# Performance work log

Hardware: AMD Instinct MI355X
Metric: run time of the kernel (lower is better)

The kernel has to match this reference:

```python
import jax, jax.numpy as jnp
import numpy as np

B, E, F, Q = 8, 2000, 6000, 20
D = 256   # entity_dim == word_dim (required: word_embedding output feeds LSTM with input_size=word_dim)
WD = 256
L = 3
NUM_ENTITY, NUM_REL, NUM_WORD = 400000, 6000, 60000
NNZ = 2 * B * F
PAGERANK_LAMBDA, FACT_SCALE = 0.8, 3.0
VERY_NEG = -100000000000.0
VERY_SMALL = 1e-10


def _lin(x, W, b):
    return x @ W.T + b


def _sparse_bmm(indices, values, x, num_rows):
    # indices: [3, nnz] = (batch, row, col); x: [B, C, Dx] -> out [B, num_rows, Dx]
    b, r, c = indices[0], indices[1], indices[2]
    contrib = values[:, None] * x[b, c]
    seg = b * num_rows + r
    out = jax.ops.segment_sum(contrib, seg, num_segments=x.shape[0] * num_rows)
    return out.reshape(x.shape[0], num_rows, x.shape[2])


def _lstm(x, Wih, Whh, bih, bhh):
    # PyTorch LSTM, batch_first, 1 layer, unidirectional; gate order i,f,g,o
    Bb, T, _ = x.shape
    H = Whh.shape[1]
    def step(carry, xt):
        h, c = carry
        g = xt @ Wih.T + bih + h @ Whh.T + bhh
        i, f, gg, o = jnp.split(g, 4, axis=-1)
        c = jax.nn.sigmoid(f) * c + jax.nn.sigmoid(i) * jnp.tanh(gg)
        h = jax.nn.sigmoid(o) * jnp.tanh(c)
        return (h, c), h
    init = (jnp.zeros((Bb, H), x.dtype), jnp.zeros((Bb, H), x.dtype))
    (h, c), hs = jax.lax.scan(step, init, jnp.swapaxes(x, 0, 1))
    return jnp.swapaxes(hs, 0, 1), h


def setup_inputs():
    key = jax.random.key(0)
    ks = iter(jax.random.split(key, 48))
    p = lambda shape: jax.random.normal(next(ks), shape, jnp.float32) * 0.02
    inp = {}
    inp['local_entity'] = jax.random.randint(next(ks), (B, E), 0, NUM_ENTITY + 1)
    inp['q2e_adj_mat'] = (jax.random.uniform(next(ks), (B, E, 1)) < 0.01).astype(jnp.float32)
    inp['kb_fact_rel'] = jax.random.randint(next(ks), (B, F), 0, NUM_REL)
    inp['query_text'] = jax.random.randint(next(ks), (B, Q), 0, NUM_WORD)
    inp['answer_dist'] = (jax.random.uniform(next(ks), (B, E)) < 0.005).astype(jnp.float32)
    eb = jax.random.randint(next(ks), (NNZ,), 0, B)
    ef = jax.random.randint(next(ks), (NNZ,), 0, F)
    ee = jax.random.randint(next(ks), (NNZ,), 0, E)
    inp['e2f_indices'] = jnp.stack([eb, ef, ee])
    inp['e2f_val'] = jnp.ones((NNZ,), jnp.float32)
    fb = jax.random.randint(next(ks), (NNZ,), 0, B)
    fe = jax.random.randint(next(ks), (NNZ,), 0, E)
    ff = jax.random.randint(next(ks), (NNZ,), 0, F)
    inp['f2e_indices'] = jnp.stack([fb, fe, ff])
    inp['f2e_val'] = jnp.ones((NNZ,), jnp.float32)
    inp['entity_table'] = p((NUM_ENTITY + 1, WD)).at[-1].set(0.0)
    inp['ent_lin_W'] = p((D, WD)); inp['ent_lin_b'] = jnp.zeros((D,), jnp.float32)
    inp['relation_table'] = p((NUM_REL + 1, WD)).at[-1].set(0.0)
    inp['rel_lin_W'] = p((D, WD)); inp['rel_lin_b'] = jnp.zeros((D,), jnp.float32)
    inp['word_table'] = p((NUM_WORD + 1, D)).at[-1].set(0.0)
    inp['lstm_Wih'] = p((4 * D, WD)); inp['lstm_Whh'] = p((4 * D, D))
    inp['lstm_bih'] = jnp.zeros((4 * D,), jnp.float32); inp['lstm_bhh'] = jnp.zeros((4 * D,), jnp.float32)
    inp['q2e_W'] = p((L, D, D)); inp['q2e_b'] = jnp.zeros((L, D), jnp.float32)
    inp['e2q_W'] = p((L, D, 3 * D)); inp['e2q_b'] = jnp.zeros((L, D), jnp.float32)
    inp['e2e_W'] = p((L, D, 3 * D)); inp['e2e_b'] = jnp.zeros((L, D), jnp.float32)
    inp['head_W'] = p((L, D, D)); inp['head_b'] = jnp.zeros((L, D), jnp.float32)
    inp['tail_W'] = p((L, D, D)); inp['tail_b'] = jnp.zeros((L, D), jnp.float32)
    inp['self_W'] = p((L, D, D)); inp['self_b'] = jnp.zeros((L, D), jnp.float32)
    inp['score_W'] = p((1, D)); inp['score_b'] = jnp.zeros((1,), jnp.float32)
    return inp


def reference(local_entity, q2e_adj_mat, kb_fact_rel, query_text, answer_dist, e2f_indices, e2f_val, f2e_indices, f2e_val, entity_table, ent_lin_W, ent_lin_b, relation_table, rel_lin_W, rel_lin_b, word_table, lstm_Wih, lstm_Whh, lstm_bih, lstm_bhh, q2e_W, q2e_b, e2q_W, e2q_b, e2e_W, e2e_b, head_W, head_b, tail_W, tail_b, self_W, self_b, score_W, score_b):
    query_mask = (query_text != NUM_WORD).astype(jnp.float32)          # [B,Q]
    local_entity_mask = (local_entity != NUM_ENTITY).astype(jnp.float32)
    # query encoder (dropout = identity in eval)
    query_hidden, h_last = _lstm(word_table[query_text], lstm_Wih, lstm_Whh, lstm_bih, lstm_bhh)
    query_node_emb = h_last[:, None, :]                                # [B,1,D]
    local_fact_emb = _lin(relation_table[kb_fact_rel], rel_lin_W, rel_lin_b)  # [B,F,D]
    div = jnp.sqrt(jnp.float32(D))
    sim = jnp.einsum('bqd,bfd->bqf', query_hidden, local_fact_emb) / div
    sim = jax.nn.softmax(sim + (1.0 - query_mask)[:, :, None] * VERY_NEG, axis=1)
    att = jnp.einsum('bqf,bqd->bfd', sim, query_hidden)
    Wt = jnp.sum(att * local_fact_emb, axis=2) / div                   # [B,F]
    W_tilde = jnp.exp(Wt - jnp.max(Wt, axis=1, keepdims=True))
    e2fT = jnp.stack([e2f_indices[0], e2f_indices[2], e2f_indices[1]])  # transpose(1,2)
    e2f_softmax = _sparse_bmm(e2fT, e2f_val, W_tilde[:, :, None], E)[..., 0]
    e2f_softmax = jnp.maximum(e2f_softmax, VERY_SMALL)
    pagerank_f = q2e_adj_mat[..., 0]                                    # [B,E]
    local_entity_emb = _lin(entity_table[local_entity], ent_lin_W, ent_lin_b)  # [B,E,D]
    for i in range(L):
        q2e_emb = jnp.broadcast_to(_lin(query_node_emb, q2e_W[i], q2e_b[i]), (B, E, D))
        nxt = jnp.concatenate([local_entity_emb, q2e_emb], axis=2)
        e2f_emb = jax.nn.relu(_lin(local_fact_emb, self_W[i], self_b[i]) + _sparse_bmm(e2f_indices, e2f_val, _lin(local_entity_emb, head_W[i], head_b[i]), F))
        e2f_norm = W_tilde[:, :, None] * _sparse_bmm(e2f_indices, e2f_val, (pagerank_f / e2f_softmax)[:, :, None], F)
        e2f_emb = e2f_emb * e2f_norm
        f2e_emb = jax.nn.relu(_lin(local_entity_emb, self_W[i], self_b[i]) + _sparse_bmm(f2e_indices, f2e_val, _lin(e2f_emb, tail_W[i], tail_b[i]), E))
        pagerank_f = PAGERANK_LAMBDA * _sparse_bmm(f2e_indices, f2e_val, e2f_norm, E)[..., 0] + (1.0 - PAGERANK_LAMBDA) * pagerank_f
        nxt = jnp.concatenate([nxt, FACT_SCALE * f2e_emb], axis=2)      # [B,E,3D]
        query_node_emb = jnp.einsum('be,bed->bd', pagerank_f, _lin(nxt, e2q_W[i], e2q_b[i]))[:, None, :]
        local_entity_emb = jax.nn.relu(_lin(nxt, e2e_W[i], e2e_b[i]))
    score = _lin(local_entity_emb, score_W, score_b)[..., 0]            # [B,E]
    loss = jnp.mean(jnp.maximum(score, 0.0) - score * answer_dist + jnp.log1p(jnp.exp(-jnp.abs(score))))
    score_m = score + (1.0 - local_entity_mask) * VERY_NEG
    pred = jnp.argmax(score_m, axis=1)
    pred_dist = jax.nn.sigmoid(score_m) * local_entity_mask
    return (loss, pred, pred_dist)
```

## Files before the change

kernel.cpp:

```cpp
#include <hip/hip_runtime.h>
#include <math.h>

#define BB 8
#define EE 2000
#define FF 6000
#define QQ 20
#define DD 256
#define NENT 400000
#define NWORD 60000
#define NNZ_ 96000
#define VNEG  (-1e11f)
#define VSMALL 1e-10f

typedef __attribute__((ext_vector_type(8))) short short8v;
typedef __attribute__((ext_vector_type(4))) short short4v;
typedef __attribute__((ext_vector_type(4))) float f32x4;

__device__ __forceinline__ unsigned short f2bf_rne(float x)
{
    unsigned u = __float_as_uint(x);
    u += 0x7FFFu + ((u >> 16) & 1u);
    return (unsigned short)(u >> 16);
}
__device__ __forceinline__ float bf2f(unsigned short h)
{
    return __uint_as_float((unsigned)h << 16);
}

template<int GATHER, int DUALW, int RELU, int RS, int BIASB>
__device__ __forceinline__ void mgemm_body(
    const float* __restrict__ A1, const int* __restrict__ idx,
    const float* __restrict__ A2, float sA2,
    const short* __restrict__ W1h, const short* __restrict__ W1l,
    const short* __restrict__ W2h, const short* __restrict__ W2l,
    const float* __restrict__ biasA,
    const float* __restrict__ rowscale, const float* __restrict__ bias2,
    float* __restrict__ out, int by, int bx,
    short* __restrict__ Ah, short* __restrict__ Al)
{
    const int tid = threadIdx.x;
    const int lane = tid & 63, wv = tid >> 6;
    const int wrow = wv >> 1, wcol = wv & 1;
    const int row0 = by * 128, col0 = bx * 64;

    const int sr = tid >> 1;
    const int sko = (tid & 1) << 5;
    const int grow = row0 + sr;
    const float* aRow1 = GATHER ? A1 + (size_t)idx[grow] * 256 : A1 + (size_t)grow * 256;
    const float* aRow2 = DUALW ? A2 + (size_t)grow * 256 : nullptr;

    f32x4 acc[4][2];
    #pragma unroll
    for (int i = 0; i < 4; ++i)
        #pragma unroll
        for (int j = 0; j < 2; ++j) acc[i][j] = (f32x4){0.f, 0.f, 0.f, 0.f};

    const int nch = DUALW ? 8 : 4;
    for (int ch = 0; ch < nch; ++ch) {
        const bool hi2 = DUALW && (ch >= 4);
        const float* ar = hi2 ? aRow2 : aRow1;
        const int kbase = (ch & 3) << 6;
        #pragma unroll
        for (int q = 0; q < 8; ++q) {
            const int kc = sko + (q << 2);
            float4 a = *(const float4*)(ar + kbase + kc);
            if (DUALW && hi2) { a.x *= sA2; a.y *= sA2; a.z *= sA2; a.w *= sA2; }
            unsigned short h0 = f2bf_rne(a.x), h1 = f2bf_rne(a.y),
                           h2 = f2bf_rne(a.z), h3 = f2bf_rne(a.w);
            unsigned short l0 = f2bf_rne(a.x - bf2f(h0)), l1 = f2bf_rne(a.y - bf2f(h1)),
                           l2 = f2bf_rne(a.z - bf2f(h2)), l3 = f2bf_rne(a.w - bf2f(h3));
            const int tI = ((sr >> 4) << 1) + (kc >> 5);
            const int off = (tI << 9) + ((((sr & 15)) + (((kc >> 3) & 3) << 4)) << 3) + (kc & 7);
            *(short4v*)(Ah + off) = (short4v){(short)h0, (short)h1, (short)h2, (short)h3};
            *(short4v*)(Al + off) = (short4v){(short)l0, (short)l1, (short)l2, (short)l3};
        }
        __syncthreads();
        const short* Wh = hi2 ? W2h : W1h;
        const short* Wl = hi2 ? W2l : W1l;
        #pragma unroll
        for (int ks = 0; ks < 2; ++ks) {
            const int kg = kbase + (ks << 5) + ((lane >> 4) << 3);
            short8v bh[2], bl[2];
            #pragma unroll
            for (int ct = 0; ct < 2; ++ct) {
                const int c = col0 + (wcol << 5) + (ct << 4) + (lane & 15);
                bh[ct] = *(const short8v*)(Wh + (size_t)c * 256 + kg);
                bl[ct] = *(const short8v*)(Wl + (size_t)c * 256 + kg);
            }
            #pragma unroll
            for (int rt = 0; rt < 4; ++rt) {
                const int tI = (((wrow << 2) + rt) << 1) + ks;
                const short8v avh = *(const short8v*)(Ah + (tI << 9) + (lane << 3));
                const short8v avl = *(const short8v*)(Al + (tI << 9) + (lane << 3));
                #pragma unroll
                for (int ct = 0; ct < 2; ++ct) {
                    acc[rt][ct] = __builtin_amdgcn_mfma_f32_16x16x32_bf16(avh, bh[ct], acc[rt][ct], 0, 0, 0);
                    acc[rt][ct] = __builtin_amdgcn_mfma_f32_16x16x32_bf16(avh, bl[ct], acc[rt][ct], 0, 0, 0);
                    acc[rt][ct] = __builtin_amdgcn_mfma_f32_16x16x32_bf16(avl, bh[ct], acc[rt][ct], 0, 0, 0);
                }
            }
        }
        __syncthreads();
    }
    #pragma unroll
    for (int rt = 0; rt < 4; ++rt) {
        const int rb = row0 + (wrow << 6) + (rt << 4) + ((lane >> 4) << 2);
        #pragma unroll
        for (int ct = 0; ct < 2; ++ct) {
            const int c = col0 + (wcol << 5) + (ct << 4) + (lane & 15);
            #pragma unroll
            for (int j = 0; j < 4; ++j) {
                const int r = rb + j;
                float v = acc[rt][ct][j];
                v += BIASB ? biasA[(size_t)(r / EE) * 256 + c] : biasA[c];
                if (RS) v += rowscale[r] * bias2[c];
                if (RELU) v = fmaxf(v, 0.f);
                out[(size_t)r * 256 + c] = v;
            }
        }
    }
}

template<int GATHER, int DUALW, int RELU, int RS, int BIASB>
__global__ __launch_bounds__(256, 2) void mgemm_k(
    const float* __restrict__ A1, const int* __restrict__ idx,
    const float* __restrict__ A2, float sA2,
    const short* __restrict__ W1h, const short* __restrict__ W1l,
    const short* __restrict__ W2h, const short* __restrict__ W2l,
    const float* __restrict__ biasA,
    const float* __restrict__ rowscale, const float* __restrict__ bias2,
    float* __restrict__ out)
{
    __shared__ short Ah[16 * 512];
    __shared__ short Al[16 * 512];
    mgemm_body<GATHER, DUALW, RELU, RS, BIASB>(A1, idx, A2, sA2, W1h, W1l, W2h, W2l,
        biasA, rowscale, bias2, out, blockIdx.y, blockIdx.x, Ah, Al);
}

__global__ __launch_bounds__(256, 2) void mgemm_pair_k(
    const float* __restrict__ Aa, const short* __restrict__ Wah, const short* __restrict__ Wal,
    const float* __restrict__ ba, float* __restrict__ outa, int nya,
    const float* __restrict__ Ab, const short* __restrict__ Wbh, const short* __restrict__ Wbl,
    const float* __restrict__ bb, float* __restrict__ outb)
{
    __shared__ short Ah[16 * 512];
    __shared__ short Al[16 * 512];
    const int by = blockIdx.y;
    if (by < nya)
        mgemm_body<0, 0, 0, 0, 0>(Aa, nullptr, nullptr, 1.f, Wah, Wal, nullptr, nullptr,
            ba, nullptr, nullptr, outa, by, blockIdx.x, Ah, Al);
    else
        mgemm_body<0, 0, 0, 0, 0>(Ab, nullptr, nullptr, 1.f, Wbh, Wbl, nullptr, nullptr,
            bb, nullptr, nullptr, outb, by - nya, blockIdx.x, Ah, Al);
}

__global__ void wpack_k(const float* __restrict__ relW, const float* __restrict__ entW,
                        const float* __restrict__ headW, const float* __restrict__ tailW,
                        const float* __restrict__ selfW, const float* __restrict__ e2eW,
                        short* __restrict__ wh, short* __restrict__ wl)
{
    int id = blockIdx.x * 256 + threadIdx.x;
    if (id >= 17 * 65536) return;
    int m = id >> 16, e = id & 65535;
    float x;
    if (m == 0)       x = relW[e];
    else if (m == 1)  x = entW[e];
    else if (m < 5)   x = headW[(size_t)(m - 2) * 65536 + e];
    else if (m < 8)   x = tailW[(size_t)(m - 5) * 65536 + e];
    else if (m < 11)  x = selfW[(size_t)(m - 8) * 65536 + e];
    else if (m < 14)  x = e2eW[(size_t)(m - 11) * 196608 + (size_t)(e >> 8) * 768 + (e & 255)];
    else              x = e2eW[(size_t)(m - 14) * 196608 + (size_t)(e >> 8) * 768 + 512 + (e & 255)];
    unsigned short h = f2bf_rne(x);
    wh[id] = (short)h;
    wl[id] = (short)f2bf_rne(x - bf2f(h));
}

template<int GATHER>
__global__ __launch_bounds__(256, 4) void gemm3_k(
    const float* __restrict__ A1, const int* __restrict__ idx,
    const float* __restrict__ W1, int ldw1,
    const float* __restrict__ biasA,
    float* __restrict__ out, int M, int N)
{
    __shared__ float As[16][68];
    __shared__ float Bs[16][132];
    const int tid = threadIdx.x;
// ... 51 lines not shown
        if (r >= M) continue;
        float* orow = out + (size_t)r * N;
        #pragma unroll
        for (int jh = 0; jh < 2; ++jh) {
            const int c = col0 + (jh << 6) + (tx << 2);
            float4 v;
            v.x = acc[i][jh * 4 + 0] + biasA[c + 0];
            v.y = acc[i][jh * 4 + 1] + biasA[c + 1];
            v.z = acc[i][jh * 4 + 2] + biasA[c + 2];
            v.w = acc[i][jh * 4 + 3] + biasA[c + 3];
            *(float4*)(orow + c) = v;
        }
    }
}

__global__ void csr_count_k(const int* __restrict__ idx, int* __restrict__ cnt, int nrPerB)
{
    int k = blockIdx.x * 256 + threadIdx.x;
    if (k >= NNZ_) return;
    atomicAdd(&cnt[idx[k] * nrPerB + idx[NNZ_ + k]], 1);
}

__global__ __launch_bounds__(1024) void scan2_k(
    const int* __restrict__ cntA, int* __restrict__ rpA, int* __restrict__ curA, int nA,
    const int* __restrict__ cntB, int* __restrict__ rpB, int* __restrict__ curB, int nB)
{
    const int* cnt = blockIdx.x ? cntB : cntA;
    int* rp  = blockIdx.x ? rpB  : rpA;
    int* cur = blockIdx.x ? curB : curA;
    int n    = blockIdx.x ? nB   : nA;
    __shared__ int sums[1024];
    int t = threadIdx.x;
    int chunk = (n + 1023) / 1024;
    int lo = t * chunk, hi = lo + chunk;
    if (lo > n) lo = n;
// ... 1 lines not shown
    int s = 0;
    for (int i = lo; i < hi; ++i) s += cnt[i];
    sums[t] = s;
    __syncthreads();
    for (int off = 1; off < 1024; off <<= 1) {
        int v = (t >= off) ? sums[t - off] : 0;
        __syncthreads();
        sums[t] += v;
        __syncthreads();
    }
    int run = (t == 0) ? 0 : sums[t - 1];
    for (int i = lo; i < hi; ++i) { rp[i] = run; cur[i] = run; run += cnt[i]; }
    if (hi == n) rp[n] = run;
}

__global__ void csr_fill_k(const int* __restrict__ idx, const float* __restrict__ val,
                           int* __restrict__ cur, int* __restrict__ col,
                           float* __restrict__ valp, int nrPerB)
{
    int k = blockIdx.x * 256 + threadIdx.x;
    if (k >= NNZ_) return;
    int row = idx[k] * nrPerB + idx[NNZ_ + k];
    int p = atomicAdd(&cur[row], 1);
    col[p] = idx[2 * NNZ_ + k];
    valp[p] = val[k];
}

__global__ void degw_k(const int* __restrict__ rp, const float* __restrict__ vp,
                       float* __restrict__ degw, int n)
{
    int r = blockIdx.x * 256 + threadIdx.x;
    if (r >= n) return;
    float s = 0.f;
    for (int j = rp[r]; j < rp[r + 1]; ++j) s += vp[j];
    degw[r] = s;
}

__global__ __launch_bounds__(256) void gather_fused_e2f_k(
    const int* __restrict__ rowptr, const int* __restrict__ col,
    const float* __restrict__ valp, const float* __restrict__ headsrc,
// ... 13 lines not shown
    int j0 = rowptr[row], j1 = rowptr[row + 1];
    for (int j = j0; j < j1; ++j) {
        int c = col[j];
        float v = valp[j];
        float4 x = *(const float4*)(headsrc + ((size_t)b * EE + c) * DD + (lane << 2));
        acc.x += v * x.x; acc.y += v * x.y; acc.z += v * x.z; acc.w += v * x.w;
        ns += v * (prb[c] / fmaxf(smb[c], VSMALL));
    }
    float nrm = Wtil[row] * ns;
    if (lane == 0) e2fnrm[row] = nrm;
    acc.x = fmaxf(acc.x, 0.f) * nrm; acc.y = fmaxf(acc.y, 0.f) * nrm;
    acc.z = fmaxf(acc.z, 0.f) * nrm; acc.w = fmaxf(acc.w, 0.f) * nrm;
    *dp = acc;
}

__global__ __launch_bounds__(256) void gather_sum_k(
    const int* __restrict__ rowptr, const int* __restrict__ col,
    const float* __restrict__ valp, const float* __restrict__ src,
    float* __restrict__ dst, int nrows, int nrPerB, int ncs)
{
    int gid = blockIdx.x * 256 + threadIdx.x;
    int row = gid >> 6, lane = gid & 63;
    if (row >= nrows) return;
    int b = row / nrPerB;
    float4 acc = make_float4(0.f, 0.f, 0.f, 0.f);
    int j0 = rowptr[row], j1 = rowptr[row + 1];
    for (int j = j0; j < j1; ++j) {
        int c = col[j];
        float v = valp[j];
        float4 x = *(const float4*)(src + ((size_t)b * ncs + c) * DD + (lane << 2));
        acc.x += v * x.x; acc.y += v * x.y; acc.z += v * x.z; acc.w += v * x.w;
    }
    *(float4*)(dst + (size_t)row * DD + (lane << 2)) = acc;
}

__global__ void transpose_whh_k(const float* __restrict__ Whh, float* __restrict__ WhhT)
{
    int i = blockIdx.x * 256 + threadIdx.x;
    int k = i >> 10, j = i & 1023;
    WhhT[i] = Whh[(size_t)j * 256 + k];
}

__global__ __launch_bounds__(256) void lstm_k(
    const float* __restrict__ Xg, const float* __restrict__ WhhT,
    const float* __restrict__ bhh, float* __restrict__ qh, float* __restrict__ qne)
{
    __shared__ float h[DD];
    __shared__ float gs[4 * DD];
// ... 55 lines not shown
        }
    }
    const float inv = 0.0625f;
    float pre[QQ], m = -INFINITY;
    #pragma unroll
    for (int q = 0; q < QQ; ++q) { pre[q] = acc[q] * inv + qmn[q]; m = fmaxf(m, pre[q]); }
    float s = 0.f;
    #pragma unroll
    for (int q = 0; q < QQ; ++q) s += expf(pre[q] - m);
    float wt = 0.f;
    #pragma unroll
    for (int q = 0; q < QQ; ++q) wt += (expf(pre[q] - m) / s) * (acc[q] * inv);
    Wt[(size_t)b * FF + f] = wt;
}

__global__ void rowmax_k(const float* __restrict__ Wt, float* __restrict__ WtMax)
{
    __shared__ float red[256];
    int b = blockIdx.x;
    float m = -INFINITY;
    for (int f = threadIdx.x; f < FF; f += 256) m = fmaxf(m, Wt[b * FF + f]);
    red[threadIdx.x] = m; __syncthreads();
    for (int s = 128; s > 0; s >>= 1) {
        if (threadIdx.x < s) red[threadIdx.x] = fmaxf(red[threadIdx.x], red[threadIdx.x + s]);
        __syncthreads();
    }
    if (threadIdx.x == 0) WtMax[b] = red[0];
}

__global__ void wtil_k(const float* __restrict__ Wt, const float* __restrict__ WtMax,
                       float* __restrict__ Wtil)
{
    int i = blockIdx.x * 256 + threadIdx.x;
    if (i >= BB * FF) return;
    Wtil[i] = expf(Wt[i] - WtMax[i / FF]);
}

__global__ void scatter_sm_k(const int* __restrict__ idx, const float* __restrict__ val,
                             const float* __restrict__ Wtil, float* __restrict__ dst)
{
    int k = blockIdx.x * 256 + threadIdx.x;
    if (k >= NNZ_) return;
    int b = idx[k], e = idx[2 * NNZ_ + k], f = idx[NNZ_ + k];
    atomicAdd(&dst[(size_t)b * EE + e], val[k] * Wtil[(size_t)b * FF + f]);
}

__global__ __launch_bounds__(256) void qlin_ebias_k(
    const float* __restrict__ qne, const float* __restrict__ q2eW,
    const float* __restrict__ q2eb, const float* __restrict__ e2eW,
    const float* __restrict__ e2eb, float* __restrict__ qlin, float* __restrict__ ebias)
// ... 90 lines not shown
    __syncthreads();
    float aq = q2ebn[j];
    const float* wq = q2eWn + (size_t)j * DD;
    #pragma unroll 4
    for (int k = 0; k < DD; ++k) aq += qn[k] * wq[k];
    qlinNext[b * DD + j] = aq;
    qs[j] = aq;
    __syncthreads();
    float ae = e2ebn[j];
    const float* we = e2eWn + (size_t)j * 768 + 256;
    #pragma unroll 4
    for (int k = 0; k < DD; ++k) ae += qs[k] * we[k];
    ebiasNext[b * DD + j] = ae;
}

__global__ void score_k(const float* __restrict__ lee, const float* __restrict__ sw,
                        const float* __restrict__ sb, float* __restrict__ score)
{
    int r = blockIdx.x * 256 + threadIdx.x;
    if (r >= BB * EE) return;
    float acc = sb[0];
    const float* a = lee + (size_t)r * DD;
    for (int k = 0; k < DD; k += 4) {
        float4 v = *(const float4*)(a + k);
        acc += v.x * sw[k] + v.y * sw[k + 1] + v.z * sw[k + 2] + v.w * sw[k + 3];
    }
    score[r] = acc;
}

__global__ __launch_bounds__(256) void final_k(
    const float* __restrict__ score, const int* __restrict__ local_entity,
    const float* __restrict__ ans, float* __restrict__ out, float* __restrict__ losspart)
{
    int b = blockIdx.x, t = threadIdx.x;
    float lsum = 0.f, bm = -INFINITY;
    int bi = EE;
    for (int e = t; e < EE; e += 256) {
        float s = score[b * EE + e];
        float mask = (local_entity[b * EE + e] != NENT) ? 1.f : 0.f;
        float smv = s + (1.f - mask) * VNEG;
        float sig;
        if (smv >= 0.f) sig = 1.f / (1.f + expf(-smv));
        else { float es = expf(smv); sig = es / (1.f + es); }
        out[1 + BB + b * EE + e] = sig * mask;
        lsum += fmaxf(s, 0.f) - s * ans[b * EE + e] + log1pf(expf(-fabsf(s)));
        if (smv > bm) { bm = smv; bi = e; }
    }
    __shared__ float rv[256]; __shared__ int ri[256]; __shared__ float rl[256];
    rv[t] = bm; ri[t] = bi; rl[t] = lsum;
    __syncthreads();
    for (int s = 128; s > 0; s >>= 1) {
        if (t < s) {
            rl[t] += rl[t + s];
// ... 49 lines not shown
    const float* head_W       = (const float*)d_in[26];
    const float* head_b       = (const float*)d_in[27];
    const float* tail_W       = (const float*)d_in[28];
    const float* tail_b       = (const float*)d_in[29];
    const float* self_W       = (const float*)d_in[30];
    const float* self_b       = (const float*)d_in[31];
    const float* score_W      = (const float*)d_in[32];
    const float* score_b      = (const float*)d_in[33];

    const int NR1 = BB * FF;
    const int NR2 = BB * EE;

    float* ws = (float*)d_ws;
    size_t off = 0;
    auto alloc = [&](size_t n) { float* p = ws + off; off += n; return p; };
    float* Xg      = alloc((size_t)BB * QQ * 1024);
    float* WhhT    = alloc((size_t)1024 * DD);
    float* qh      = alloc((size_t)BB * QQ * DD);
    float* qne     = alloc(BB * DD);
    float* lfe     = alloc((size_t)NR1 * DD);
    float* lee     = alloc((size_t)NR2 * DD);
    float* lee2    = alloc((size_t)NR2 * DD);
    float* Wt      = alloc(BB * FF);
    float* WtMax   = alloc(8);
    float* Wtil    = alloc(BB * FF);
    float* e2fsm   = alloc(BB * EE);
    float* pr      = alloc(BB * EE);
    float* qlinA   = alloc(BB * DD);
    float* qlinB   = alloc(BB * DD);
    float* ebiasA  = alloc(BB * DD);
    float* ebiasB  = alloc(BB * DD);
    float* e2fnrm  = alloc(BB * FF);
    float* scoreb  = alloc(BB * EE);
    float* losspart= alloc(8);
    float* bufC    = alloc((size_t)NR2 * DD);
    float* e2fT    = alloc((size_t)NR1 * DD);
    float* f2eT    = alloc((size_t)NR2 * DD);
    float* tmp     = alloc((size_t)NR2 * DD);
    float* vpartL  = alloc((size_t)NCHK * BB * DD);
    float* vpartF  = alloc((size_t)NCHK * BB * DD);
    float* vpartS  = alloc(NCHK * BB);
    float* degw2   = alloc(NR2);
    float* e2f_vp  = alloc(NNZ_);
    float* f2e_vp  = alloc(NNZ_);
    short* wbh = (short*)alloc(17 * 65536 / 2);
    short* wbl = (short*)alloc(17 * 65536 / 2);
    int* ib = (int*)(ws + off);
    size_t ioff = 0;
    auto ialloc = [&](size_t n) { int* p = ib + ioff; ioff += n; return p; };
    int* e2f_cnt = ialloc(NR1);
    int* e2f_rp  = ialloc(NR1 + 1);
    int* e2f_cur = ialloc(NR1);
    int* e2f_col = ialloc(NNZ_);
    int* f2e_cnt = ialloc(NR2);
    int* f2e_rp  = ialloc(NR2 + 1);
    int* f2e_cur = ialloc(NR2);
    int* f2e_col = ialloc(NNZ_);

    auto WH = [&](int m) { return wbh + (size_t)m * 65536; };
    auto WL = [&](int m) { return wbl + (size_t)m * 65536; };

    float* outp = (float*)d_out;
    const int SCB = (NNZ_ + 255) / 256;

    wpack_k<<<(17 * 65536) / 256, 256, 0, stream>>>(rel_W, ent_W, head_W, tail_W,
                                                    self_W, e2e_W, wbh, wbl);

    hipMemsetAsync(e2f_cnt, 0, NR1 * sizeof(int), stream);
    hipMemsetAsync(f2e_cnt, 0, NR2 * sizeof(int), stream);
    csr_count_k<<<SCB, 256, 0, stream>>>(e2f_idx, e2f_cnt, FF);
    csr_count_k<<<SCB, 256, 0, stream>>>(f2e_idx, f2e_cnt, EE);
    scan2_k<<<2, 1024, 0, stream>>>(e2f_cnt, e2f_rp, e2f_cur, NR1,
                                    f2e_cnt, f2e_rp, f2e_cur, NR2);
    csr_fill_k<<<SCB, 256, 0, stream>>>(e2f_idx, e2f_val, e2f_cur, e2f_col, e2f_vp, FF);
    csr_fill_k<<<SCB, 256, 0, stream>>>(f2e_idx, f2e_val, f2e_cur, f2e_col, f2e_vp, EE);
    degw_k<<<(NR2 + 255) / 256, 256, 0, stream>>>(f2e_rp, f2e_vp, degw2, NR2);

    gemm3_k<1><<<dim3(8, 3), 256, 0, stream>>>(
        word_table, query_text, Wih, 256, bih, Xg, BB * QQ, 1024);
    transpose_whh_k<<<1024, 256, 0, stream>>>(Whh, WhhT);
    lstm_k<<<BB, 256, 0, stream>>>(Xg, WhhT, bhh, qh, qne);

    mgemm_k<1, 0, 0, 0, 0><<<dim3(4, 375), 256, 0, stream>>>(
        rel_table, kb_fact_rel, nullptr, 1.f, WH(0), WL(0), nullptr, nullptr,
        rel_b, nullptr, nullptr, lfe);
    mgemm_k<1, 0, 0, 0, 0><<<dim3(4, 125), 256, 0, stream>>>(
        entity_table, local_entity, nullptr, 1.f, WH(1), WL(1), nullptr, nullptr,
        ent_b, nullptr, nullptr, lee);

    simwt_k<<<dim3((FF + 255) / 256, BB), 256, 0, stream>>>(qh, query_text, lfe, Wt);
    rowmax_k<<<BB, 256, 0, stream>>>(Wt, WtMax);
    wtil_k<<<(BB * FF + 255) / 256, 256, 0, stream>>>(Wt, WtMax, Wtil);

    hipMemsetAsync(e2fsm, 0, BB * EE * sizeof(float), stream);
    scatter_sm_k<<<SCB, 256, 0, stream>>>(e2f_idx, e2f_val, Wtil, e2fsm);

    hipMemcpyAsync(pr, q2e_adj, BB * EE * sizeof(float), hipMemcpyDeviceToDevice, stream);
    qlin_ebias_k<<<BB, 256, 0, stream>>>(qne, q2e_W, q2e_b, e2e_W, e2e_b, qlinA, ebiasA);

    float* qlinCur = qlinA;  float* qlinNxt = qlinB;
    float* ebiasCur = ebiasA; float* ebiasNxt = ebiasB;

    for (int i = 0; i < 3; ++i) {
        const float* e2qWi  = e2q_W  + (size_t)i * DD * 3 * DD;
        const float* e2qbi  = e2q_b  + i * DD;
        const float* headbi = head_b + i * DD;
        const float* tailbi = tail_b + i * DD;
        const float* selfbi = self_b + i * DD;

        mgemm_pair_k<<<dim3(4, 125 + 375), 256, 0, stream>>>(
            lee, WH(2 + i), WL(2 + i), headbi, bufC, 125,
            lfe, WH(8 + i), WL(8 + i), selfbi, e2fT);

        gather_fused_e2f_k<<<(NR1 * 64) / 256, 256, 0, stream>>>(
            e2f_rp, e2f_col, e2f_vp, bufC, pr, e2fsm, Wtil, e2fnrm, e2fT, NR1);

        gather_sum_k<<<(NR2 * 64) / 256, 256, 0, stream>>>(
            f2e_rp, f2e_col, f2e_vp, e2fT, tmp, NR2, EE, FF);

        mgemm_k<0, 1, 1, 1, 0><<<dim3(4, 125), 256, 0, stream>>>(
            lee, nullptr, tmp, 1.f, WH(8 + i), WL(8 + i), WH(5 + i), WL(5 + i),
            selfbi, degw2, tailbi, f2eT);

        vreduce_pr_k<<<dim3(NCHK, BB), 256, 0, stream>>>(
            f2e_rp, f2e_col, f2e_vp, e2fnrm, pr, lee, f2eT, vpartL, vpartF, vpartS);

        int hasNext = (i < 2) ? 1 : 0;
        const float* q2eWn = q2e_W + (size_t)(i + 1) * DD * DD * (hasNext ? 1 : 0);
        const float* q2ebn = q2e_b + (i + 1) * DD * (hasNext ? 1 : 0);
        const float* e2eWn = e2e_W + (size_t)(i + 1) * DD * 3 * DD * (hasNext ? 1 : 0);
        const float* e2ebn = e2e_b + (i + 1) * DD * (hasNext ? 1 : 0);
        qneupd_qlin_k<<<BB, 256, 0, stream>>>(
            vpartL, vpartF, vpartS, qlinCur, e2qWi, e2qbi, qne,
            q2eWn, q2ebn, e2eWn, e2ebn, qlinNxt, ebiasNxt, hasNext);

        mgemm_k<0, 1, 1, 0, 1><<<dim3(4, 125), 256, 0, stream>>>(
            lee, nullptr, f2eT, 3.f, WH(11 + i), WL(11 + i), WH(14 + i), WL(14 + i),
            ebiasCur, nullptr, nullptr, lee2);
        { float* t = lee; lee = lee2; lee2 = t; }
        { float* t = qlinCur; qlinCur = qlinNxt; qlinNxt = t; }
        { float* t = ebiasCur; ebiasCur = ebiasNxt; ebiasNxt = t; }
    }

    score_k<<<(BB * EE + 255) / 256, 256, 0, stream>>>(lee, score_W, score_b, scoreb);
    final_k<<<BB, 256, 0, stream>>>(scoreb, local_entity, answer_dist, outp, losspart);
    loss_k<<<1, 64, 0, stream>>>(losspart, outp);
}
```

Baseline: 1.295 ms.

## Pre-split GEMM activations into bf16 hi/lo buffers and drop LDS staging

The GEMM kernels stop converting fp32 activations to bf16 hi/lo pairs inside every tile. Producers (a row-gather split kernel, gather_sum, and the GEMM epilogues) now write hi/lo bf16 copies once, and the new GEMM reads MFMA operands straight from global memory with no shared memory or barriers, using a 64x128 tile. The 3x scale on the f2e operand moves into the packed weights. Several small kernels are also merged (CSR count/fill, rowmax+wtil, score+final). This trades repeated conversion and LDS traffic for extra global bf16 buffers, uncoalesced direct operand loads and extra epilogue stores.

```diff
diff --git a/kernel.cpp b/kernel.cpp
--- a/kernel.cpp
+++ b/kernel.cpp
@@ -27,27 +27,22 @@
     return __uint_as_float((unsigned)h << 16);
 }
 
-template<int GATHER, int DUALW, int RELU, int RS, int BIASB>
-__device__ __forceinline__ void mgemm_body(
-    const float* __restrict__ A1, const int* __restrict__ idx,
-    const float* __restrict__ A2, float sA2,
+template<int DUALW, int RELU, int RS, int BIASB, int WRITEB>
+__device__ __forceinline__ void mgemm2_body(
+    const short* __restrict__ Ah1, const short* __restrict__ Al1,
+    const short* __restrict__ Ah2, const short* __restrict__ Al2,
     const short* __restrict__ W1h, const short* __restrict__ W1l,
     const short* __restrict__ W2h, const short* __restrict__ W2l,
     const float* __restrict__ biasA,
     const float* __restrict__ rowscale, const float* __restrict__ bias2,
-    float* __restrict__ out, int by, int bx,
-    short* __restrict__ Ah, short* __restrict__ Al)
+    float* __restrict__ outF, short* __restrict__ outH, short* __restrict__ outL,
+    int by, int bx)
 {
     const int tid = threadIdx.x;
-    const int lane = tid & 63, wv = tid >> 6;
-    const int wrow = wv >> 1, wcol = wv & 1;
-    const int row0 = by * 128, col0 = bx * 64;
-
-    const int sr = tid >> 1;
-    const int sko = (tid & 1) << 5;
-    const int grow = row0 + sr;
-    const float* aRow1 = GATHER ? A1 + (size_t)idx[grow] * 256 : A1 + (size_t)grow * 256;
-    const float* aRow2 = DUALW ? A2 + (size_t)grow * 256 : nullptr;
+    const int lane = tid & 63, w = tid >> 6;
+    const int row0 = by * 64, col0 = bx * 128 + w * 32;
+    const int rA = row0 + (lane & 15);
+    const int kofs = (lane >> 4) << 3;
 
     f32x4 acc[4][2];
     #pragma unroll
@@ -55,59 +50,41 @@
         #pragma unroll
         for (int j = 0; j < 2; ++j) acc[i][j] = (f32x4){0.f, 0.f, 0.f, 0.f};
 
-    const int nch = DUALW ? 8 : 4;
-    for (int ch = 0; ch < nch; ++ch) {
-        const bool hi2 = DUALW && (ch >= 4);
-        const float* ar = hi2 ? aRow2 : aRow1;
-        const int kbase = (ch & 3) << 6;
+    const int nks = DUALW ? 16 : 8;
+    #pragma unroll 2
+    for (int ks = 0; ks < nks; ++ks) {
+        const bool hi2 = DUALW && (ks >= 8);
+        const short* __restrict__ AH = hi2 ? Ah2 : Ah1;
+        const short* __restrict__ AL = hi2 ? Al2 : Al1;
+        const short* __restrict__ WH = hi2 ? W2h : W1h;
+        const short* __restrict__ WL = hi2 ? W2l : W1l;
+        const int kg = ((ks & 7) << 5) + kofs;
+        const size_t b0 = (size_t)(col0 + (lane & 15)) * 256 + kg;
+        const size_t b1 = (size_t)(col0 + 16 + (lane & 15)) * 256 + kg;
+        short8v bh0 = *(const short8v*)(WH + b0);
+        short8v bh1 = *(const short8v*)(WH + b1);
+        short8v bl0 = *(const short8v*)(WL + b0);
+        short8v bl1 = *(const short8v*)(WL + b1);
         #pragma unroll
-        for (int q = 0; q < 8; ++q) {
-            const int kc = sko + (q << 2);
-            float4 a = *(const float4*)(ar + kbase + kc);
-            if (DUALW && hi2) { a.x *= sA2; a.y *= sA2; a.z *= sA2; a.w *= sA2; }
-            unsigned short h0 = f2bf_rne(a.x), h1 = f2bf_rne(a.y),
-                           h2 = f2bf_rne(a.z), h3 = f2bf_rne(a.w);
-            unsigned short l0 = f2bf_rne(a.x - bf2f(h0)), l1 = f2bf_rne(a.y - bf2f(h1)),
-                           l2 = f2bf_rne(a.z - bf2f(h2)), l3 = f2bf_rne(a.w - bf2f(h3));
-            const int tI = ((sr >> 4) << 1) + (kc >> 5);
-            const int off = (tI << 9) + ((((sr & 15)) + (((kc >> 3) & 3) << 4)) << 3) + (kc & 7);
-            *(short4v*)(Ah + off) = (short4v){(short)h0, (short)h1, (short)h2, (short)h3};
-            *(short4v*)(Al + off) = (short4v){(short)l0, (short)l1, (short)l2, (short)l3};
+        for (int rt = 0; rt < 4; ++rt) {
+            const size_t aoff = (size_t)(rA + (rt << 4)) * 256 + kg;
+            short8v avh = *(const short8v*)(AH + aoff);
+            short8v avl = *(const short8v*)(AL + aoff);
+            acc[rt][0] = __builtin_amdgcn_mfma_f32_16x16x32_bf16(avh, bh0, acc[rt][0], 0, 0, 0);
+            acc[rt][0] = __builtin_amdgcn_mfma_f32_16x16x32_bf16(avh, bl0, acc[rt][0], 0, 0, 0);
+            acc[rt][0] = __builtin_amdgcn_mfma_f32_16x16x32_bf16(avl, bh0, acc[rt][0], 0, 0, 0);
+            acc[rt][1] = __builtin_amdgcn_mfma_f32_16x16x32_bf16(avh, bh1, acc[rt][1], 0, 0, 0);
+            acc[rt][1] = __builtin_amdgcn_mfma_f32_16x16x32_bf16(avh, bl1, acc[rt][1], 0, 0, 0);
+            acc[rt][1] = __builtin_amdgcn_mfma_f32_16x16x32_bf16(avl, bh1, acc[rt][1], 0, 0, 0);
         }
-        __syncthreads();
-        const short* Wh = hi2 ? W2h : W1h;
-        const short* Wl = hi2 ? W2l : W1l;
-        #pragma unroll
-        for (int ks = 0; ks < 2; ++ks) {
-            const int kg = kbase + (ks << 5) + ((lane >> 4) << 3);
-            short8v bh[2], bl[2];
-            #pragma unroll
-            for (int ct = 0; ct < 2; ++ct) {
-                const int c = col0 + (wcol << 5) + (ct << 4) + (lane & 15);
-                bh[ct] = *(const short8v*)(Wh + (size_t)c * 256 + kg);
-                bl[ct] = *(const short8v*)(Wl + (size_t)c * 256 + kg);
-            }
-            #pragma unroll
-            for (int rt = 0; rt < 4; ++rt) {
-                const int tI = (((wrow << 2) + rt) << 1) + ks;
-                const short8v avh = *(const short8v*)(Ah + (tI << 9) + (lane << 3));
-                const short8v avl = *(const short8v*)(Al + (tI << 9) + (lane << 3));
-                #pragma unroll
-                for (int ct = 0; ct < 2; ++ct) {
-                    acc[rt][ct] = __builtin_amdgcn_mfma_f32_16x16x32_bf16(avh, bh[ct], acc[rt][ct], 0, 0, 0);
-                    acc[rt][ct] = __builtin_amdgcn_mfma_f32_16x16x32_bf16(avh, bl[ct], acc[rt][ct], 0, 0, 0);
-                    acc[rt][ct] = __builtin_amdgcn_mfma_f32_16x16x32_bf16(avl, bh[ct], acc[rt][ct], 0, 0, 0);
-                }
-            }
-        }
-        __syncthreads();
-    }
+    }
+
     #pragma unroll
     for (int rt = 0; rt < 4; ++rt) {
-        const int rb = row0 + (wrow << 6) + (rt << 4) + ((lane >> 4) << 2);
+        const int rb = row0 + (rt << 4) + ((lane >> 4) << 2);
         #pragma unroll
         for (int ct = 0; ct < 2; ++ct) {
-            const int c = col0 + (wcol << 5) + (ct << 4) + (lane & 15);
+            const int c = col0 + (ct << 4) + (lane & 15);
             #pragma unroll
             for (int j = 0; j < 4; ++j) {
                 const int r = rb + j;
@@ -115,43 +92,76 @@
                 v += BIASB ? biasA[(size_t)(r / EE) * 256 + c] : biasA[c];
                 if (RS) v += rowscale[r] * bias2[c];
                 if (RELU) v = fmaxf(v, 0.f);
-                out[(size_t)r * 256 + c] = v;
+                outF[(size_t)r * 256 + c] = v;
+                if (WRITEB) {
+                    unsigned short h = f2bf_rne(v);
+                    outH[(size_t)r * 256 + c] = (short)h;
+                    outL[(size_t)r * 256 + c] = (short)f2bf_rne(v - bf2f(h));
+                }
             }
         }
     }
 }
 
-template<int GATHER, int DUALW, int RELU, int RS, int BIASB>
-__global__ __launch_bounds__(256, 2) void mgemm_k(
-    const float* __restrict__ A1, const int* __restrict__ idx,
-    const float* __restrict__ A2, float sA2,
+template<int DUALW, int RELU, int RS, int BIASB, int WRITEB>
+__global__ __launch_bounds__(256) void mgemm2_k(
+    const short* __restrict__ Ah1, const short* __restrict__ Al1,
+    const short* __restrict__ Ah2, const short* __restrict__ Al2,
     const short* __restrict__ W1h, const short* __restrict__ W1l,
     const short* __restrict__ W2h, const short* __restrict__ W2l,
     const float* __restrict__ biasA,
     const float* __restrict__ rowscale, const float* __restrict__ bias2,
-    float* __restrict__ out)
-{
-    __shared__ short Ah[16 * 512];
-    __shared__ short Al[16 * 512];
-    mgemm_body<GATHER, DUALW, RELU, RS, BIASB>(A1, idx, A2, sA2, W1h, W1l, W2h, W2l,
-        biasA, rowscale, bias2, out, blockIdx.y, blockIdx.x, Ah, Al);
-}
-
-__global__ __launch_bounds__(256, 2) void mgemm_pair_k(
-    const float* __restrict__ Aa, const short* __restrict__ Wah, const short* __restrict__ Wal,
-    const float* __restrict__ ba, float* __restrict__ outa, int nya,
-    const float* __restrict__ Ab, const short* __restrict__ Wbh, const short* __restrict__ Wbl,
-    const float* __restrict__ bb, float* __restrict__ outb)
-{
-    __shared__ short Ah[16 * 512];
-    __shared__ short Al[16 * 512];
+    float* __restrict__ outF, short* __restrict__ outH, short* __restrict__ outL)
+{
+    mgemm2_body<DUALW, RELU, RS, BIASB, WRITEB>(Ah1, Al1, Ah2, Al2, W1h, W1l, W2h, W2l,
+        biasA, rowscale, bias2, outF, outH, outL, blockIdx.y, blockIdx.x);
+}
+
+template<int WRITEB>
+__global__ __launch_bounds__(256) void mgemm2_pair_k(
+    const short* __restrict__ AhA, const short* __restrict__ AlA,
+    const short* __restrict__ WhA, const short* __restrict__ WlA,
+    const float* __restrict__ bA, float* __restrict__ outFA,
+    short* __restrict__ outHA, short* __restrict__ outLA, int nya,
+    const short* __restrict__ AhB, const short* __restrict__ AlB,
+    const short* __restrict__ WhB, const short* __restrict__ WlB,
+    const float* __restrict__ bB, float* __restrict__ outFB,
+    short* __restrict__ outHB, short* __restrict__ outLB)
+{
     const int by = blockIdx.y;
     if (by < nya)
-        mgemm_body<0, 0, 0, 0, 0>(Aa, nullptr, nullptr, 1.f, Wah, Wal, nullptr, nullptr,
-            ba, nullptr, nullptr, outa, by, blockIdx.x, Ah, Al);
+        mgemm2_body<0, 0, 0, 0, WRITEB>(AhA, AlA, nullptr, nullptr, WhA, WlA,
+            nullptr, nullptr, bA, nullptr, nullptr, outFA, outHA, outLA, by, blockIdx.x);
     else
-        mgemm_body<0, 0, 0, 0, 0>(Ab, nullptr, nullptr, 1.f, Wbh, Wbl, nullptr, nullptr,
-            bb, nullptr, nullptr, outb, by - nya, blockIdx.x, Ah, Al);
+        mgemm2_body<0, 0, 0, 0, WRITEB>(AhB, AlB, nullptr, nullptr, WhB, WlB,
+            nullptr, nullptr, bB, nullptr, nullptr, outFB, outHB, outLB, by - nya, blockIdx.x);
+}
+
+__global__ __launch_bounds__(256) void split_rows_k(
+    const float* __restrict__ rel_table, const int* __restrict__ kb_fact_rel,
+    const float* __restrict__ ent_table, const int* __restrict__ local_entity,
+    short* __restrict__ relH, short* __restrict__ relL,
+    short* __restrict__ entH, short* __restrict__ entL)
+{
+    int rw = blockIdx.x * 4 + (threadIdx.x >> 6);
+    int lane = threadIdx.x & 63;
+    const float* src;
+    short *dh, *dl;
+    size_t drow;
+    if (rw < 48000) {
+        src = rel_table + (size_t)kb_fact_rel[rw] * 256;
+        dh = relH; dl = relL; drow = (size_t)rw * 256;
+    } else {
+        int r = rw - 48000;
+        src = ent_table + (size_t)local_entity[r] * 256;
+        dh = entH; dl = entL; drow = (size_t)r * 256;
+    }
+    float4 a = *(const float4*)(src + (lane << 2));
+    unsigned short h0 = f2bf_rne(a.x), h1 = f2bf_rne(a.y), h2 = f2bf_rne(a.z), h3 = f2bf_rne(a.w);
+    *(short4v*)(dh + drow + (lane << 2)) = (short4v){(short)h0, (short)h1, (short)h2, (short)h3};
+    *(short4v*)(dl + drow + (lane << 2)) = (short4v){
+        (short)f2bf_rne(a.x - bf2f(h0)), (short)f2bf_rne(a.y - bf2f(h1)),
+        (short)f2bf_rne(a.z - bf2f(h2)), (short)f2bf_rne(a.w - bf2f(h3))};
 }
 
 __global__ void wpack_k(const float* __restrict__ relW, const float* __restrict__ entW,
@@ -169,7 +179,7 @@
     else if (m < 8)   x = tailW[(size_t)(m - 5) * 65536 + e];
     else if (m < 11)  x = selfW[(size_t)(m - 8) * 65536 + e];
     else if (m < 14)  x = e2eW[(size_t)(m - 11) * 196608 + (size_t)(e >> 8) * 768 + (e & 255)];
-    else              x = e2eW[(size_t)(m - 14) * 196608 + (size_t)(e >> 8) * 768 + 512 + (e & 255)];
+    else              x = 3.f * e2eW[(size_t)(m - 14) * 196608 + (size_t)(e >> 8) * 768 + 512 + (e & 255)];
     unsigned short h = f2bf_rne(x);
     wh[id] = (short)h;
     wl[id] = (short)f2bf_rne(x - bf2f(h));
@@ -251,11 +261,13 @@
     }
 }
 
-__global__ void csr_count_k(const int* __restrict__ idx, int* __restrict__ cnt, int nrPerB)
+__global__ void csr_count2_k(const int* __restrict__ idxA, int* __restrict__ cntA,
+                             const int* __restrict__ idxB, int* __restrict__ cntB)
 {
     int k = blockIdx.x * 256 + threadIdx.x;
     if (k >= NNZ_) return;
-    atomicAdd(&cnt[idx[k] * nrPerB + idx[NNZ_ + k]], 1);
+    if (blockIdx.y == 0) atomicAdd(&cntA[idxA[k] * FF + idxA[NNZ_ + k]], 1);
+    else                 atomicAdd(&cntB[idxB[k] * EE + idxB[NNZ_ + k]], 1);
 }
 
 __global__ __launch_bounds__(1024) void scan2_k(
@@ -287,16 +299,25 @@
     if (hi == n) rp[n] = run;
 }
 
-__global__ void csr_fill_k(const int* __restrict__ idx, const float* __restrict__ val,
-                           int* __restrict__ cur, int* __restrict__ col,
-                           float* __restrict__ valp, int nrPerB)
+__global__ void csr_fill2_k(
+    const int* __restrict__ idxA, const float* __restrict__ valA,
+    int* __restrict__ curA, int* __restrict__ colA, float* __restrict__ vpA,
+    const int* __restrict__ idxB, const float* __restrict__ valB,
+    int* __restrict__ curB, int* __restrict__ colB, float* __restrict__ vpB)
 {
     int k = blockIdx.x * 256 + threadIdx.x;
     if (k >= NNZ_) return;
-    int row = idx[k] * nrPerB + idx[NNZ_ + k];
-    int p = atomicAdd(&cur[row], 1);
-    col[p] = idx[2 * NNZ_ + k];
-    valp[p] = val[k];
+    if (blockIdx.y == 0) {
+        int row = idxA[k] * FF + idxA[NNZ_ + k];
+        int p = atomicAdd(&curA[row], 1);
+        colA[p] = idxA[2 * NNZ_ + k];
+        vpA[p] = valA[k];
+    } else {
+        int row = idxB[k] * EE + idxB[NNZ_ + k];
+        int p = atomicAdd(&curB[row], 1);
+        colB[p] = idxB[2 * NNZ_ + k];
+        vpB[p] = valB[k];
+    }
 }
 
 __global__ void degw_k(const int* __restrict__ rp, const float* __restrict__ vp,
@@ -340,10 +361,10 @@
     *dp = acc;
 }
 
-__global__ __launch_bounds__(256) void gather_sum_k(
+__global__ __launch_bounds__(256) void gather_sum_bf_k(
     const int* __restrict__ rowptr, const int* __restrict__ col,
     const float* __restrict__ valp, const float* __restrict__ src,
-    float* __restrict__ dst, int nrows, int nrPerB, int ncs)
+    short* __restrict__ dh, short* __restrict__ dl, int nrows, int nrPerB, int ncs)
 {
     int gid = blockIdx.x * 256 + threadIdx.x;
     int row = gid >> 6, lane = gid & 63;
@@ -357,7 +378,13 @@
         float4 x = *(const float4*)(src + ((size_t)b * ncs + c) * DD + (lane << 2));
         acc.x += v * x.x; acc.y += v * x.y; acc.z += v * x.z; acc.w += v * x.w;
     }
-    *(float4*)(dst + (size_t)row * DD + (lane << 2)) = acc;
+    unsigned short h0 = f2bf_rne(acc.x), h1 = f2bf_rne(acc.y),
+                   h2 = f2bf_rne(acc.z), h3 = f2bf_rne(acc.w);
+    size_t o = (size_t)row * DD + (lane << 2);
+    *(short4v*)(dh + o) = (short4v){(short)h0, (short)h1, (short)h2, (short)h3};
+    *(short4v*)(dl + o) = (short4v){
+        (short)f2bf_rne(acc.x - bf2f(h0)), (short)f2bf_rne(acc.y - bf2f(h1)),
+        (short)f2bf_rne(acc.z - bf2f(h2)), (short)f2bf_rne(acc.w - bf2f(h3))};
 }
 
 __global__ void transpose_whh_k(const float* __restrict__ Whh, float* __restrict__ WhhT)
@@ -443,26 +470,20 @@
     Wt[(size_t)b * FF + f] = wt;
 }
 
-__global__ void rowmax_k(const float* __restrict__ Wt, float* __restrict__ WtMax)
+__global__ __launch_bounds__(256) void rowmax_wtil_k(
+    const float* __restrict__ Wt, float* __restrict__ Wtil)
 {
     __shared__ float red[256];
-    int b = blockIdx.x;
+    int b = blockIdx.x, t = threadIdx.x;
     float m = -INFINITY;
-    for (int f = threadIdx.x; f < FF; f += 256) m = fmaxf(m, Wt[b * FF + f]);
-    red[threadIdx.x] = m; __syncthreads();
+    for (int f = t; f < FF; f += 256) m = fmaxf(m, Wt[b * FF + f]);
+    red[t] = m; __syncthreads();
     for (int s = 128; s > 0; s >>= 1) {
-        if (threadIdx.x < s) red[threadIdx.x] = fmaxf(red[threadIdx.x], red[threadIdx.x + s]);
+        if (t < s) red[t] = fmaxf(red[t], red[t + s]);
         __syncthreads();
     }
-    if (threadIdx.x == 0) WtMax[b] = red[0];
-}
-
-__global__ void wtil_k(const float* __restrict__ Wt, const float* __restrict__ WtMax,
-                       float* __restrict__ Wtil)
-{
-    int i = blockIdx.x * 256 + threadIdx.x;
-    if (i >= BB * FF) return;
-    Wtil[i] = expf(Wt[i] - WtMax[i / FF]);
+    float mx = red[0];
+    for (int f = t; f < FF; f += 256) Wtil[b * FF + f] = expf(Wt[b * FF + f] - mx);
 }
 
 __global__ void scatter_sm_k(const int* __restrict__ idx, const float* __restrict__ val,
@@ -583,29 +604,25 @@
     ebiasNext[b * DD + j] = ae;
 }
 
-__global__ void score_k(const float* __restrict__ lee, const float* __restrict__ sw,
-                        const float* __restrict__ sb, float* __restrict__ score)
-{
-    int r = blockIdx.x * 256 + threadIdx.x;
-    if (r >= BB * EE) return;
-    float acc = sb[0];
-    const float* a = lee + (size_t)r * DD;
-    for (int k = 0; k < DD; k += 4) {
-        float4 v = *(const float4*)(a + k);
-        acc += v.x * sw[k] + v.y * sw[k + 1] + v.z * sw[k + 2] + v.w * sw[k + 3];
-    }
-    score[r] = acc;
-}
-
-__global__ __launch_bounds__(256) void final_k(
-    const float* __restrict__ score, const int* __restrict__ local_entity,
+__global__ __launch_bounds__(256) void final2_k(
+    const float* __restrict__ lee, const float* __restrict__ sw_,
+    const float* __restrict__ sb, const int* __restrict__ local_entity,
     const float* __restrict__ ans, float* __restrict__ out, float* __restrict__ losspart)
 {
+    __shared__ float sw[DD];
     int b = blockIdx.x, t = threadIdx.x;
+    sw[t] = sw_[t];
+    __syncthreads();
+    float sb0 = sb[0];
     float lsum = 0.f, bm = -INFINITY;
     int bi = EE;
     for (int e = t; e < EE; e += 256) {
-        float s = score[b * EE + e];
+        const float* a = lee + ((size_t)b * EE + e) * DD;
+        float s = sb0;
+        for (int k = 0; k < DD; k += 4) {
+            float4 v = *(const float4*)(a + k);
+            s += v.x * sw[k] + v.y * sw[k + 1] + v.z * sw[k + 2] + v.w * sw[k + 3];
+        }
         float mask = (local_entity[b * EE + e] != NENT) ? 1.f : 0.f;
         float smv = s + (1.f - mask) * VNEG;
         float sig;
@@ -685,15 +702,15 @@
     float* ws = (float*)d_ws;
     size_t off = 0;
     auto alloc = [&](size_t n) { float* p = ws + off; off += n; return p; };
+    auto salloc = [&](size_t nshorts) { short* p = (short*)(ws + off); off += nshorts / 2; return p; };
     float* Xg      = alloc((size_t)BB * QQ * 1024);
     float* WhhT    = alloc((size_t)1024 * DD);
     float* qh      = alloc((size_t)BB * QQ * DD);
     float* qne     = alloc(BB * DD);
     float* lfe     = alloc((size_t)NR1 * DD);
-    float* lee     = alloc((size_t)NR2 * DD);
-    float* lee2    = alloc((size_t)NR2 * DD);
+    float* leeA    = alloc((size_t)NR2 * DD);
+    float* leeB    = alloc((size_t)NR2 * DD);
     float* Wt      = alloc(BB * FF);
-    float* WtMax   = alloc(8);
     float* Wtil    = alloc(BB * FF);
     float* e2fsm   = alloc(BB * EE);
     float* pr      = alloc(BB * EE);
@@ -702,20 +719,32 @@
     float* ebiasA  = alloc(BB * DD);
     float* ebiasB  = alloc(BB * DD);
     float* e2fnrm  = alloc(BB * FF);
-    float* scoreb  = alloc(BB * EE);
     float* losspart= alloc(8);
     float* bufC    = alloc((size_t)NR2 * DD);
     float* e2fT    = alloc((size_t)NR1 * DD);
     float* f2eT    = alloc((size_t)NR2 * DD);
-    float* tmp     = alloc((size_t)NR2 * DD);
     float* vpartL  = alloc((size_t)NCHK * BB * DD);
     float* vpartF  = alloc((size_t)NCHK * BB * DD);
     float* vpartS  = alloc(NCHK * BB);
     float* degw2   = alloc(NR2);
     float* e2f_vp  = alloc(NNZ_);
     float* f2e_vp  = alloc(NNZ_);
-    short* wbh = (short*)alloc(17 * 65536 / 2);
-    short* wbl = (short*)alloc(17 * 65536 / 2);
+    short* relH  = salloc((size_t)NR1 * DD);
+    short* relL  = salloc((size_t)NR1 * DD);
+    short* entH  = salloc((size_t)NR2 * DD);
+    short* entL  = salloc((size_t)NR2 * DD);
+    short* lfeH  = salloc((size_t)NR1 * DD);
+    short* lfeL  = salloc((size_t)NR1 * DD);
+    short* leeHA = salloc((size_t)NR2 * DD);
+    short* leeLA = salloc((size_t)NR2 * DD);
+    short* leeHB = salloc((size_t)NR2 * DD);
+    short* leeLB = salloc((size_t)NR2 * DD);
+    short* f2eH  = salloc((size_t)NR2 * DD);
+    short* f2eL  = salloc((size_t)NR2 * DD);
+    short* tmpH  = salloc((size_t)NR2 * DD);
+    short* tmpL  = salloc((size_t)NR2 * DD);
+    short* wbh   = salloc((size_t)17 * 65536);
+    short* wbl   = salloc((size_t)17 * 65536);
     int* ib = (int*)(ws + off);
     size_t ioff = 0;
     auto ialloc = [&](size_t n) { int* p = ib + ioff; ioff += n; return p; };
@@ -736,15 +765,17 @@
 
     wpack_k<<<(17 * 65536) / 256, 256, 0, stream>>>(rel_W, ent_W, head_W, tail_W,
                                                     self_W, e2e_W, wbh, wbl);
+    split_rows_k<<<(NR1 + NR2) / 4, 256, 0, stream>>>(
+        rel_table, kb_fact_rel, entity_table, local_entity, relH, relL, entH, entL);
 
     hipMemsetAsync(e2f_cnt, 0, NR1 * sizeof(int), stream);
     hipMemsetAsync(f2e_cnt, 0, NR2 * sizeof(int), stream);
-    csr_count_k<<<SCB, 256, 0, stream>>>(e2f_idx, e2f_cnt, FF);
-    csr_count_k<<<SCB, 256, 0, stream>>>(f2e_idx, f2e_cnt, EE);
+    csr_count2_k<<<dim3(SCB, 2), 256, 0, stream>>>(e2f_idx, e2f_cnt, f2e_idx, f2e_cnt);
     scan2_k<<<2, 1024, 0, stream>>>(e2f_cnt, e2f_rp, e2f_cur, NR1,
                                     f2e_cnt, f2e_rp, f2e_cur, NR2);
-    csr_fill_k<<<SCB, 256, 0, stream>>>(e2f_idx, e2f_val, e2f_cur, e2f_col, e2f_vp, FF);
-    csr_fill_k<<<SCB, 256, 0, stream>>>(f2e_idx, f2e_val, f2e_cur, f2e_col, f2e_vp, EE);
+    csr_fill2_k<<<dim3(SCB, 2), 256, 0, stream>>>(
+        e2f_idx, e2f_val, e2f_cur, e2f_col, e2f_vp,
+        f2e_idx, f2e_val, f2e_cur, f2e_col, f2e_vp);
     degw_k<<<(NR2 + 255) / 256, 256, 0, stream>>>(f2e_rp, f2e_vp, degw2, NR2);
 
     gemm3_k<1><<<dim3(8, 3), 256, 0, stream>>>(
@@ -752,16 +783,12 @@
     transpose_whh_k<<<1024, 256, 0, stream>>>(Whh, WhhT);
     lstm_k<<<BB, 256, 0, stream>>>(Xg, WhhT, bhh, qh, qne);
 
-    mgemm_k<1, 0, 0, 0, 0><<<dim3(4, 375), 256, 0, stream>>>(
-        rel_table, kb_fact_rel, nullptr, 1.f, WH(0), WL(0), nullptr, nullptr,
-        rel_b, nullptr, nullptr, lfe);
-    mgemm_k<1, 0, 0, 0, 0><<<dim3(4, 125), 256, 0, stream>>>(
-        entity_table, local_entity, nullptr, 1.f, WH(1), WL(1), nullptr, nullptr,
-        ent_b, nullptr, nullptr, lee);
+    mgemm2_pair_k<1><<<dim3(2, 750 + 250), 256, 0, stream>>>(
+        relH, relL, WH(0), WL(0), rel_b, lfe, lfeH, lfeL, 750,
+        entH, entL, WH(1), WL(1), ent_b, leeA, leeHA, leeLA);
 
     simwt_k<<<dim3((FF + 255) / 256, BB), 256, 0, stream>>>(qh, query_text, lfe, Wt);
-    rowmax_k<<<BB, 256, 0, stream>>>(Wt, WtMax);
-    wtil_k<<<(BB * FF + 255) / 256, 256, 0, stream>>>(Wt, WtMax, Wtil);
+    rowmax_wtil_k<<<BB, 256, 0, stream>>>(Wt, Wtil);
 
     hipMemsetAsync(e2fsm, 0, BB * EE * sizeof(float), stream);
     scatter_sm_k<<<SCB, 256, 0, stream>>>(e2f_idx, e2f_val, Wtil, e2fsm);
@@ -769,6 +796,9 @@
     hipMemcpyAsync(pr, q2e_adj, BB * EE * sizeof(float), hipMemcpyDeviceToDevice, stream);
     qlin_ebias_k<<<BB, 256, 0, stream>>>(qne, q2e_W, q2e_b, e2e_W, e2e_b, qlinA, ebiasA);
 
+    float* lee = leeA;   float* lee2 = leeB;
+    short* leeH = leeHA; short* leeL = leeLA;
+    short* leeH2 = leeHB; short* leeL2 = leeLB;
     float* qlinCur = qlinA;  float* qlinNxt = qlinB;
     float* ebiasCur = ebiasA; float* ebiasNxt = ebiasB;
 
@@ -779,19 +809,19 @@
         const float* tailbi = tail_b + i * DD;
         const float* selfbi = self_b + i * DD;
 
-        mgemm_pair_k<<<dim3(4, 125 + 375), 256, 0, stream>>>(
-            lee, WH(2 + i), WL(2 + i), headbi, bufC, 125,
-            lfe, WH(8 + i), WL(8 + i), selfbi, e2fT);
+        mgemm2_pair_k<0><<<dim3(2, 250 + 750), 256, 0, stream>>>(
+            leeH, leeL, WH(2 + i), WL(2 + i), headbi, bufC, nullptr, nullptr, 250,
+            lfeH, lfeL, WH(8 + i), WL(8 + i), selfbi, e2fT, nullptr, nullptr);
 
         gather_fused_e2f_k<<<(NR1 * 64) / 256, 256, 0, stream>>>(
             e2f_rp, e2f_col, e2f_vp, bufC, pr, e2fsm, Wtil, e2fnrm, e2fT, NR1);
 
-        gather_sum_k<<<(NR2 * 64) / 256, 256, 0, stream>>>(
-            f2e_rp, f2e_col, f2e_vp, e2fT, tmp, NR2, EE, FF);
-
-        mgemm_k<0, 1, 1, 1, 0><<<dim3(4, 125), 256, 0, stream>>>(
-            lee, nullptr, tmp, 1.f, WH(8 + i), WL(8 + i), WH(5 + i), WL(5 + i),
-            selfbi, degw2, tailbi, f2eT);
+        gather_sum_bf_k<<<(NR2 * 64) / 256, 256, 0, stream>>>(
+            f2e_rp, f2e_col, f2e_vp, e2fT, tmpH, tmpL, NR2, EE, FF);
+
+        mgemm2_k<1, 1, 1, 0, 1><<<dim3(2, 250), 256, 0, stream>>>(
+            leeH, leeL, tmpH, tmpL, WH(8 + i), WL(8 + i), WH(5 + i), WL(5 + i),
+            selfbi, degw2, tailbi, f2eT, f2eH, f2eL);
 
         vreduce_pr_k<<<dim3(NCHK, BB), 256, 0, stream>>>(
             f2e_rp, f2e_col, f2e_vp, e2fnrm, pr, lee, f2eT, vpartL, vpartF, vpartS);
@@ -805,15 +835,17 @@
             vpartL, vpartF, vpartS, qlinCur, e2qWi, e2qbi, qne,
             q2eWn, q2ebn, e2eWn, e2ebn, qlinNxt, ebiasNxt, hasNext);
 
-        mgemm_k<0, 1, 1, 0, 1><<<dim3(4, 125), 256, 0, stream>>>(
-            lee, nullptr, f2eT, 3.f, WH(11 + i), WL(11 + i), WH(14 + i), WL(14 + i),
-            ebiasCur, nullptr, nullptr, lee2);
+        mgemm2_k<1, 1, 0, 1, 1><<<dim3(2, 250), 256, 0, stream>>>(
+            leeH, leeL, f2eH, f2eL, WH(11 + i), WL(11 + i), WH(14 + i), WL(14 + i),
+            ebiasCur, nullptr, nullptr, lee2, leeH2, leeL2);
         { float* t = lee; lee = lee2; lee2 = t; }
+        { short* t = leeH; leeH = leeH2; leeH2 = t; }
+        { short* t = leeL; leeL = leeL2; leeL2 = t; }
         { float* t = qlinCur; qlinCur = qlinNxt; qlinNxt = t; }
         { float* t = ebiasCur; ebiasCur = ebiasNxt; ebiasNxt = t; }
     }
 
-    score_k<<<(BB * EE + 255) / 256, 256, 0, stream>>>(lee, score_W, score_b, scoreb);
-    final_k<<<BB, 256, 0, stream>>>(scoreb, local_entity, answer_dist, outp, losspart);
+    final2_k<<<BB, 256, 0, stream>>>(lee, score_W, score_b, local_entity,
+                                     answer_dist, outp, losspart);
     loss_k<<<1, 64, 0, stream>>>(losspart, outp);
 }
```

Result: slower. 1.554 ms (+20.0%).
